# Kernel optimization log

Measured on AMD Instinct MI355X. Metric: run time of the kernel, lower is better.

The kernel has to match this reference:

```python
import jax, jax.numpy as jnp
import numpy as np

NEG_BIG = -1e9


def setup_inputs() -> dict:
    key = jax.random.key(0)
    ks = jax.random.split(key, 6)
    B, Tq, Tv, D, A = 4, 256, 1024, 512, 128
    inputs = jax.random.normal(ks[0], (B, Tv, D), dtype=jnp.float32)
    context = jax.random.normal(ks[1], (B, Tq, D), dtype=jnp.float32)
    mask = jnp.ones((B, Tv), dtype=jnp.int32)  # 1 = valid position
    scale = 1.0 / np.sqrt(D)
    Wk = jax.random.normal(ks[2], (D, A), dtype=jnp.float32) * scale
    bk = jnp.zeros((A,), dtype=jnp.float32)
    Wq = jax.random.normal(ks[3], (D, A), dtype=jnp.float32) * scale
    bq = jnp.zeros((A,), dtype=jnp.float32)
    attn_v = jax.random.normal(ks[4], (A,), dtype=jnp.float32) * (1.0 / np.sqrt(A))
    return {"inputs": inputs, "context": context, "mask": mask,
            "Wk": Wk, "bk": bk, "Wq": Wq, "bq": bq, "attn_v": attn_v}


def reference(inputs, context, mask, Wk, bk, Wq, bq, attn_v):
    # inputs: [B,Tv,D] (keys/values), context: [B,Tq,D] (queries)
    k = jnp.einsum('bvd,da->bva', inputs, Wk) + bk        # [B,Tv,A]
    q = jnp.einsum('bqd,da->bqa', context, Wq) + bq       # [B,Tq,A]
    # additive (Bahdanau) score: sum_a v_a * tanh(q + k)
    t = jnp.tanh(q[:, :, None, :] + k[:, None, :, :])     # [B,Tq,Tv,A]
    scores = jnp.einsum('bqva,a->bqv', t, attn_v)         # [B,Tq,Tv]
    neg = (1.0 - mask.astype(jnp.float32))[:, None, :] * NEG_BIG
    scores = scores + neg
    attn = jax.nn.softmax(scores, axis=-1)                # [B,Tq,Tv]
    return jnp.einsum('bqv,bvd->bqd', attn, inputs)       # [B,Tq,D]
```

## Files before the change

kernel.cpp:

```cpp
#include <hip/hip_runtime.h>
#include <math.h>

#define B   4
#define TQ  256
#define TV  1024
#define D   512
#define A   128

#define LOG2E     1.4426950408889634f
#define TWO_LOG2E 2.8853900817779268f
#define NEG_BIG_F (-1e9f)

#define QBLK (B * TQ / 8)
#define KBLK (B * TV / 8)

__global__ __launch_bounds__(512, 4) void proj_exp_kernel(
    const float* __restrict__ ctx, const float* __restrict__ inp,
    const float* __restrict__ Wq, const float* __restrict__ bq,
    const float* __restrict__ Wk, const float* __restrict__ bk,
    float* __restrict__ Eq, float* __restrict__ EkT) {
  __shared__ float ps[8][8][A];
  __shared__ float es[A][9];

  bool isQ = blockIdx.x < QBLK;
  const float* X; const float* W; const float* bias; int r0;
  if (isQ) { X = ctx; W = Wq; bias = bq; r0 = blockIdx.x * 8; }
  else     { X = inp; W = Wk; bias = bk; r0 = (blockIdx.x - QBLK) * 8; }

  int tid = threadIdx.x;
  int ap = (tid & 63) * 2;
  int g  = tid >> 6;

  int dbase = __builtin_amdgcn_readfirstlane(g * 64);
  const float* Xr = X + (size_t)r0 * D + dbase;
  const float* Wd = W + (size_t)dbase * A + ap;

  float2 acc[8];
#pragma unroll
  for (int j = 0; j < 8; ++j) acc[j] = make_float2(0.f, 0.f);

#pragma unroll 2
  for (int dd = 0; dd < 64; dd += 4) {
    float2 w0 = *(const float2*)(Wd + (size_t)(dd + 0) * A);
    float2 w1 = *(const float2*)(Wd + (size_t)(dd + 1) * A);
    float2 w2 = *(const float2*)(Wd + (size_t)(dd + 2) * A);
    float2 w3 = *(const float2*)(Wd + (size_t)(dd + 3) * A);
    float4 x[8];
#pragma unroll
    for (int j = 0; j < 8; ++j)
      x[j] = *(const float4*)(Xr + (size_t)j * D + dd);
#pragma unroll
    for (int j = 0; j < 8; ++j) {
      acc[j].x = fmaf(x[j].x, w0.x, acc[j].x);
      acc[j].y = fmaf(x[j].x, w0.y, acc[j].y);
      acc[j].x = fmaf(x[j].y, w1.x, acc[j].x);
      acc[j].y = fmaf(x[j].y, w1.y, acc[j].y);
      acc[j].x = fmaf(x[j].z, w2.x, acc[j].x);
      acc[j].y = fmaf(x[j].z, w2.y, acc[j].y);
      acc[j].x = fmaf(x[j].w, w3.x, acc[j].x);
      acc[j].y = fmaf(x[j].w, w3.y, acc[j].y);
    }
  }

#pragma unroll
  for (int j = 0; j < 8; ++j)
    *(float2*)&ps[j][g][ap] = acc[j];
  __syncthreads();

  int j  = tid >> 6;
  int a2 = (tid & 63) * 2;
  float2 s0 = *(const float2*)&ps[j][0][a2];
  float2 s1 = *(const float2*)&ps[j][1][a2];
  float2 s2 = *(const float2*)&ps[j][2][a2];
  float2 s3 = *(const float2*)&ps[j][3][a2];
  float2 s4 = *(const float2*)&ps[j][4][a2];
  float2 s5 = *(const float2*)&ps[j][5][a2];
  float2 s6 = *(const float2*)&ps[j][6][a2];
  float2 s7 = *(const float2*)&ps[j][7][a2];
  float2 bz = *(const float2*)(bias + a2);
  float2 ev;
  ev.x = __builtin_amdgcn_exp2f(
      ((((s0.x + s1.x) + (s2.x + s3.x)) + ((s4.x + s5.x) + (s6.x + s7.x))) + bz.x) * TWO_LOG2E);
  ev.y = __builtin_amdgcn_exp2f(
      ((((s0.y + s1.y) + (s2.y + s3.y)) + ((s4.y + s5.y) + (s6.y + s7.y))) + bz.y) * TWO_LOG2E);

  if (isQ) {
    *(float2*)(Eq + (size_t)(r0 + j) * A + a2) = ev;
  } else {
    es[a2 + 0][j] = ev.x;
    es[a2 + 1][j] = ev.y;
    __syncthreads();
    int b  = r0 >> 10;
    int v0 = r0 & (TV - 1);
    for (int i = tid; i < A * 8; i += 512) {
      int aa = i >> 3, jj = i & 7;
      EkT[((size_t)b * A + aa) * TV + v0 + jj] = es[aa][jj];
    }
  }
}

__global__ __launch_bounds__(1024, 4) void score_softmax_kernel(
    const float* __restrict__ Eq, const float* __restrict__ EkT,
    const float* __restrict__ attn_v, const int* __restrict__ mask,
    float* __restrict__ attn) {
  __shared__ float red[4][16];
  __shared__ float bc[8];

  int tid = threadIdx.x;
  int v0  = tid;
  int xcd = blockIdx.x & 7;
  int b   = xcd & 3;
  int quad = (xcd >> 2) * 32 + (blockIdx.x >> 3);
  int r0  = b * TQ + quad * 4;

  const float* eq0 = Eq + (size_t)(r0 + 0) * A;
  const float* eq1 = Eq + (size_t)(r0 + 1) * A;
  const float* eq2 = Eq + (size_t)(r0 + 2) * A;
  const float* eq3 = Eq + (size_t)(r0 + 3) * A;

  float sumV = 0.f;
#pragma unroll 16
  for (int i = 0; i < A; ++i) sumV += attn_v[i];

  const float* ekb = EkT + (size_t)b * A * TV + v0;
  float t[4] = {0.f, 0.f, 0.f, 0.f};

  float c[4], n[4];
#pragma unroll
  for (int aa = 0; aa < 4; ++aa) c[aa] = ekb[(size_t)aa * TV];

  for (int i = 0; i < A; i += 4) {
    if (i < A - 4) {
#pragma unroll
      for (int aa = 0; aa < 4; ++aa) n[aa] = ekb[(size_t)(i + 4 + aa) * TV];
    }
#pragma unroll
    for (int aa = 0; aa < 4; ++aa) {
      float av = attn_v[i + aa];
      float q0v = eq0[i + aa], q1v = eq1[i + aa];
      float q2v = eq2[i + aa], q3v = eq3[i + aa];
      t[0] = fmaf(av, __builtin_amdgcn_rcpf(fmaf(c[aa], q0v, 1.f)), t[0]);
      t[1] = fmaf(av, __builtin_amdgcn_rcpf(fmaf(c[aa], q1v, 1.f)), t[1]);
      t[2] = fmaf(av, __builtin_amdgcn_rcpf(fmaf(c[aa], q2v, 1.f)), t[2]);
      t[3] = fmaf(av, __builtin_amdgcn_rcpf(fmaf(c[aa], q3v, 1.f)), t[3]);
    }
#pragma unroll
    for (int aa = 0; aa < 4; ++aa) c[aa] = n[aa];
  }

  int mk = mask[b * TV + v0];
  float mkv = (1.f - (float)mk) * NEG_BIG_F;
  float s[4];
#pragma unroll
  for (int r = 0; r < 4; ++r) s[r] = sumV - 2.f * t[r] + mkv;

  float m[4];
#pragma unroll
  for (int r = 0; r < 4; ++r) m[r] = s[r];
  for (int off = 32; off > 0; off >>= 1) {
#pragma unroll
    for (int r = 0; r < 4; ++r) m[r] = fmaxf(m[r], __shfl_down(m[r], off, 64));
  }
  int w = tid >> 6;
  if ((tid & 63) == 0) {
#pragma unroll
    for (int r = 0; r < 4; ++r) red[r][w] = m[r];
  }
  __syncthreads();
  if (tid < 4) {
    float a = red[tid][0];
#pragma unroll
    for (int i = 1; i < 16; ++i) a = fmaxf(a, red[tid][i]);
    bc[tid] = a;
  }
  __syncthreads();
  float M0 = bc[0], M1 = bc[1], M2 = bc[2], M3 = bc[3];

  float e[4];
  e[0] = __builtin_amdgcn_exp2f((s[0] - M0) * LOG2E);
  e[1] = __builtin_amdgcn_exp2f((s[1] - M1) * LOG2E);
  e[2] = __builtin_amdgcn_exp2f((s[2] - M2) * LOG2E);
  e[3] = __builtin_amdgcn_exp2f((s[3] - M3) * LOG2E);
  float l[4];
#pragma unroll
  for (int r = 0; r < 4; ++r) l[r] = e[r];
  for (int off = 32; off > 0; off >>= 1) {
#pragma unroll
    for (int r = 0; r < 4; ++r) l[r] += __shfl_down(l[r], off, 64);
  }
  __syncthreads();
  if ((tid & 63) == 0) {
#pragma unroll
    for (int r = 0; r < 4; ++r) red[r][w] = l[r];
  }
  __syncthreads();
  if (tid < 4) {
    float a = 0.f;
#pragma unroll
    for (int i = 0; i < 16; ++i) a += red[tid][i];
    bc[4 + tid] = a;
  }
  __syncthreads();
  float i0 = 1.f / bc[4], i1 = 1.f / bc[5], i2 = 1.f / bc[6], i3 = 1.f / bc[7];

  attn[(size_t)(r0 + 0) * TV + v0] = e[0] * i0;
  attn[(size_t)(r0 + 1) * TV + v0] = e[1] * i1;
  attn[(size_t)(r0 + 2) * TV + v0] = e[2] * i2;
  attn[(size_t)(r0 + 3) * TV + v0] = e[3] * i3;
}

__global__ __launch_bounds__(512, 4) void pv_kernel(
    const float* __restrict__ attn, const float* __restrict__ X,
    float* __restrict__ out) {
  __shared__ float lds[8 * 1024];
  int gsl = blockIdx.x & 15;
  int b   = gsl & 3;
  int dt  = gsl >> 2;
  int qt  = blockIdx.x >> 4;
  int q0  = b * TQ + qt * 8;
  int tid  = threadIdx.x;
  int w    = tid >> 6;
  int lane = tid & 63;
  int col  = lane & 31;
  int qh   = lane >> 5;
  int d0 = dt * 128 + col * 4;

  float4 acc[4];
#pragma unroll
  for (int j = 0; j < 4; ++j) acc[j] = make_float4(0.f, 0.f, 0.f, 0.f);

  int vbase = w * 128;
  const float* Xb = X + ((size_t)b * TV + vbase) * D + d0;
  const float* arow = attn + (size_t)(q0 + qh * 4) * TV + vbase;

  float4 xc0 = *(const float4*)(Xb + (size_t)0 * D);
  float4 xc1 = *(const float4*)(Xb + (size_t)1 * D);
  float4 xc2 = *(const float4*)(Xb + (size_t)2 * D);
  float4 xc3 = *(const float4*)(Xb + (size_t)3 * D);
  float4 ac[4], an[4];
#pragma unroll
  for (int j = 0; j < 4; ++j)
    ac[j] = *(const float4*)(arow + (size_t)j * TV);

  for (int vi = 0; vi < 128; vi += 4) {
    float4 xn0, xn1, xn2, xn3;
    if (vi < 124) {
      const float* Xn = Xb + (size_t)(vi + 4) * D;
      xn0 = *(const float4*)(Xn + (size_t)0 * D);
      xn1 = *(const float4*)(Xn + (size_t)1 * D);
      xn2 = *(const float4*)(Xn + (size_t)2 * D);
      xn3 = *(const float4*)(Xn + (size_t)3 * D);
#pragma unroll
      for (int j = 0; j < 4; ++j)
        an[j] = *(const float4*)(arow + (size_t)j * TV + vi + 4);
    }
#pragma unroll
    for (int j = 0; j < 4; ++j) {
      float4 av = ac[j];
      acc[j].x = fmaf(av.x, xc0.x, acc[j].x);
      acc[j].y = fmaf(av.x, xc0.y, acc[j].y);
      acc[j].z = fmaf(av.x, xc0.z, acc[j].z);
      acc[j].w = fmaf(av.x, xc0.w, acc[j].w);
      acc[j].x = fmaf(av.y, xc1.x, acc[j].x);
      acc[j].y = fmaf(av.y, xc1.y, acc[j].y);
      acc[j].z = fmaf(av.y, xc1.z, acc[j].z);
      acc[j].w = fmaf(av.y, xc1.w, acc[j].w);
      acc[j].x = fmaf(av.z, xc2.x, acc[j].x);
      acc[j].y = fmaf(av.z, xc2.y, acc[j].y);
      acc[j].z = fmaf(av.z, xc2.z, acc[j].z);
      acc[j].w = fmaf(av.z, xc2.w, acc[j].w);
      acc[j].x = fmaf(av.w, xc3.x, acc[j].x);
      acc[j].y = fmaf(av.w, xc3.y, acc[j].y);
      acc[j].z = fmaf(av.w, xc3.z, acc[j].z);
      acc[j].w = fmaf(av.w, xc3.w, acc[j].w);
    }
    xc0 = xn0; xc1 = xn1; xc2 = xn2; xc3 = xn3;
#pragma unroll
    for (int j = 0; j < 4; ++j) ac[j] = an[j];
  }

  {
    float4* pat = (float4*)lds + (size_t)w * 256;
#pragma unroll
    for (int j = 0; j < 4; ++j)
      pat[(qh * 4 + j) * 32 + col] = acc[j];
  }
  __syncthreads();

  if (tid < 256) {
    int row = tid >> 5;
    int c   = tid & 31;
    const float4* p = (const float4*)lds + tid;
    float4 r = p[0];
#pragma unroll
    for (int i = 1; i < 8; ++i) {
      float4 t = p[(size_t)i * 256];
      r.x += t.x; r.y += t.y; r.z += t.z; r.w += t.w;
    }
    *(float4*)(out + (size_t)(q0 + row) * D + dt * 128 + c * 4) = r;
  }
}

extern "C" void kernel_launch(void* const* d_in, const int* in_sizes, int n_in,
                              void* d_out, int out_size, void* d_ws, size_t ws_size,
                              hipStream_t stream) {
  const float* inputs  = (const float*)d_in[0];
  const float* context = (const float*)d_in[1];
  const int*   mask    = (const int*)d_in[2];
  const float* Wk      = (const float*)d_in[3];
  const float* bk      = (const float*)d_in[4];
  const float* Wq      = (const float*)d_in[5];
  const float* bq      = (const float*)d_in[6];
  const float* attn_v  = (const float*)d_in[7];
  float* out = (float*)d_out;

  float* Eq   = (float*)d_ws;
  float* EkT  = Eq + B * TQ * A;
  float* attn = EkT + (size_t)B * A * TV;

  proj_exp_kernel<<<QBLK + KBLK, 512, 0, stream>>>(context, inputs, Wq, bq,
                                                   Wk, bk, Eq, EkT);
  score_softmax_kernel<<<B * TQ / 4, 1024, 0, stream>>>(Eq, EkT, attn_v, mask,
                                                        attn);
  pv_kernel<<<512, 512, 0, stream>>>(attn, inputs, out);
}
```

Measured before the change: 146.8 us.

## Halve score block threads with float2 per thread; stage attn rows in LDS for PV

The score/softmax kernel now runs 512 threads per block, and each thread handles two adjacent key positions with float2 loads and stores, so every query value it loads feeds twice as many tanh evaluations. The PV kernel copies the block's 8 attention rows into LDS with a cooperative load and then reads them from LDS instead of issuing strided global loads per thread. Risks: the score kernel has fewer waves in flight to hide latency, and the PV kernel adds an extra barrier plus LDS read traffic in its inner loop.

```diff
diff --git a/kernel.cpp b/kernel.cpp
--- a/kernel.cpp
+++ b/kernel.cpp
@@ -99,15 +99,15 @@
   }
 }
 
-__global__ __launch_bounds__(1024, 4) void score_softmax_kernel(
+__global__ __launch_bounds__(512, 4) void score_softmax_kernel(
     const float* __restrict__ Eq, const float* __restrict__ EkT,
     const float* __restrict__ attn_v, const int* __restrict__ mask,
     float* __restrict__ attn) {
-  __shared__ float red[4][16];
+  __shared__ float red[4][8];
   __shared__ float bc[8];
 
   int tid = threadIdx.x;
-  int v0  = tid;
+  int v0  = (tid & 63) * 2 + (tid >> 6) * 128;
   int xcd = blockIdx.x & 7;
   int b   = xcd & 3;
   int quad = (xcd >> 2) * 32 + (blockIdx.x >> 3);
@@ -123,40 +123,54 @@
   for (int i = 0; i < A; ++i) sumV += attn_v[i];
 
   const float* ekb = EkT + (size_t)b * A * TV + v0;
-  float t[4] = {0.f, 0.f, 0.f, 0.f};
-
-  float c[4], n[4];
-#pragma unroll
-  for (int aa = 0; aa < 4; ++aa) c[aa] = ekb[(size_t)aa * TV];
+  float2 t0 = make_float2(0.f, 0.f);
+  float2 t1 = make_float2(0.f, 0.f);
+  float2 t2 = make_float2(0.f, 0.f);
+  float2 t3 = make_float2(0.f, 0.f);
+
+  float2 c0 = *(const float2*)(ekb + (size_t)0 * TV);
+  float2 c1 = *(const float2*)(ekb + (size_t)1 * TV);
+  float2 c2 = *(const float2*)(ekb + (size_t)2 * TV);
+  float2 c3 = *(const float2*)(ekb + (size_t)3 * TV);
 
   for (int i = 0; i < A; i += 4) {
+    float2 n0, n1, n2, n3;
     if (i < A - 4) {
-#pragma unroll
-      for (int aa = 0; aa < 4; ++aa) n[aa] = ekb[(size_t)(i + 4 + aa) * TV];
+      n0 = *(const float2*)(ekb + (size_t)(i + 4) * TV);
+      n1 = *(const float2*)(ekb + (size_t)(i + 5) * TV);
+      n2 = *(const float2*)(ekb + (size_t)(i + 6) * TV);
+      n3 = *(const float2*)(ekb + (size_t)(i + 7) * TV);
     }
 #pragma unroll
     for (int aa = 0; aa < 4; ++aa) {
-      float av = attn_v[i + aa];
+      float2 c = (aa == 0) ? c0 : (aa == 1) ? c1 : (aa == 2) ? c2 : c3;
+      float av  = attn_v[i + aa];
       float q0v = eq0[i + aa], q1v = eq1[i + aa];
       float q2v = eq2[i + aa], q3v = eq3[i + aa];
-      t[0] = fmaf(av, __builtin_amdgcn_rcpf(fmaf(c[aa], q0v, 1.f)), t[0]);
-      t[1] = fmaf(av, __builtin_amdgcn_rcpf(fmaf(c[aa], q1v, 1.f)), t[1]);
-      t[2] = fmaf(av, __builtin_amdgcn_rcpf(fmaf(c[aa], q2v, 1.f)), t[2]);
-      t[3] = fmaf(av, __builtin_amdgcn_rcpf(fmaf(c[aa], q3v, 1.f)), t[3]);
-    }
-#pragma unroll
-    for (int aa = 0; aa < 4; ++aa) c[aa] = n[aa];
-  }
-
-  int mk = mask[b * TV + v0];
-  float mkv = (1.f - (float)mk) * NEG_BIG_F;
-  float s[4];
-#pragma unroll
-  for (int r = 0; r < 4; ++r) s[r] = sumV - 2.f * t[r] + mkv;
+      t0.x = fmaf(av, __builtin_amdgcn_rcpf(fmaf(c.x, q0v, 1.f)), t0.x);
+      t0.y = fmaf(av, __builtin_amdgcn_rcpf(fmaf(c.y, q0v, 1.f)), t0.y);
+      t1.x = fmaf(av, __builtin_amdgcn_rcpf(fmaf(c.x, q1v, 1.f)), t1.x);
+      t1.y = fmaf(av, __builtin_amdgcn_rcpf(fmaf(c.y, q1v, 1.f)), t1.y);
+      t2.x = fmaf(av, __builtin_amdgcn_rcpf(fmaf(c.x, q2v, 1.f)), t2.x);
+      t2.y = fmaf(av, __builtin_amdgcn_rcpf(fmaf(c.y, q2v, 1.f)), t2.y);
+      t3.x = fmaf(av, __builtin_amdgcn_rcpf(fmaf(c.x, q3v, 1.f)), t3.x);
+      t3.y = fmaf(av, __builtin_amdgcn_rcpf(fmaf(c.y, q3v, 1.f)), t3.y);
+    }
+    c0 = n0; c1 = n1; c2 = n2; c3 = n3;
+  }
+
+  int2 mk = *(const int2*)(mask + b * TV + v0);
+  float mkx = (1.f - (float)mk.x) * NEG_BIG_F;
+  float mky = (1.f - (float)mk.y) * NEG_BIG_F;
+  float2 s[4];
+  s[0].x = sumV - 2.f * t0.x + mkx;  s[0].y = sumV - 2.f * t0.y + mky;
+  s[1].x = sumV - 2.f * t1.x + mkx;  s[1].y = sumV - 2.f * t1.y + mky;
+  s[2].x = sumV - 2.f * t2.x + mkx;  s[2].y = sumV - 2.f * t2.y + mky;
+  s[3].x = sumV - 2.f * t3.x + mkx;  s[3].y = sumV - 2.f * t3.y + mky;
 
   float m[4];
 #pragma unroll
-  for (int r = 0; r < 4; ++r) m[r] = s[r];
+  for (int r = 0; r < 4; ++r) m[r] = fmaxf(s[r].x, s[r].y);
   for (int off = 32; off > 0; off >>= 1) {
 #pragma unroll
     for (int r = 0; r < 4; ++r) m[r] = fmaxf(m[r], __shfl_down(m[r], off, 64));
@@ -170,20 +184,20 @@
   if (tid < 4) {
     float a = red[tid][0];
 #pragma unroll
-    for (int i = 1; i < 16; ++i) a = fmaxf(a, red[tid][i]);
+    for (int i = 1; i < 8; ++i) a = fmaxf(a, red[tid][i]);
     bc[tid] = a;
   }
   __syncthreads();
-  float M0 = bc[0], M1 = bc[1], M2 = bc[2], M3 = bc[3];
-
-  float e[4];
-  e[0] = __builtin_amdgcn_exp2f((s[0] - M0) * LOG2E);
-  e[1] = __builtin_amdgcn_exp2f((s[1] - M1) * LOG2E);
-  e[2] = __builtin_amdgcn_exp2f((s[2] - M2) * LOG2E);
-  e[3] = __builtin_amdgcn_exp2f((s[3] - M3) * LOG2E);
+  float M[4] = {bc[0], bc[1], bc[2], bc[3]};
+
+  float2 e[4];
   float l[4];
 #pragma unroll
-  for (int r = 0; r < 4; ++r) l[r] = e[r];
+  for (int r = 0; r < 4; ++r) {
+    e[r].x = __builtin_amdgcn_exp2f((s[r].x - M[r]) * LOG2E);
+    e[r].y = __builtin_amdgcn_exp2f((s[r].y - M[r]) * LOG2E);
+    l[r] = e[r].x + e[r].y;
+  }
   for (int off = 32; off > 0; off >>= 1) {
 #pragma unroll
     for (int r = 0; r < 4; ++r) l[r] += __shfl_down(l[r], off, 64);
@@ -197,16 +211,17 @@
   if (tid < 4) {
     float a = 0.f;
 #pragma unroll
-    for (int i = 0; i < 16; ++i) a += red[tid][i];
+    for (int i = 0; i < 8; ++i) a += red[tid][i];
     bc[4 + tid] = a;
   }
   __syncthreads();
-  float i0 = 1.f / bc[4], i1 = 1.f / bc[5], i2 = 1.f / bc[6], i3 = 1.f / bc[7];
-
-  attn[(size_t)(r0 + 0) * TV + v0] = e[0] * i0;
-  attn[(size_t)(r0 + 1) * TV + v0] = e[1] * i1;
-  attn[(size_t)(r0 + 2) * TV + v0] = e[2] * i2;
-  attn[(size_t)(r0 + 3) * TV + v0] = e[3] * i3;
+
+#pragma unroll
+  for (int r = 0; r < 4; ++r) {
+    float inv = 1.f / bc[4 + r];
+    *(float2*)(attn + (size_t)(r0 + r) * TV + v0) =
+        make_float2(e[r].x * inv, e[r].y * inv);
+  }
 }
 
 __global__ __launch_bounds__(512, 4) void pv_kernel(
@@ -225,22 +240,25 @@
   int qh   = lane >> 5;
   int d0 = dt * 128 + col * 4;
 
+  {
+    const float4* src = (const float4*)(attn + (size_t)q0 * TV);
+    float4* dst = (float4*)lds;
+    for (int i = tid; i < 8 * 256; i += 512) dst[i] = src[i];
+  }
+  __syncthreads();
+
   float4 acc[4];
 #pragma unroll
   for (int j = 0; j < 4; ++j) acc[j] = make_float4(0.f, 0.f, 0.f, 0.f);
 
   int vbase = w * 128;
   const float* Xb = X + ((size_t)b * TV + vbase) * D + d0;
-  const float* arow = attn + (size_t)(q0 + qh * 4) * TV + vbase;
+  const float* arow = &lds[(qh * 4) * 1024 + vbase];
 
   float4 xc0 = *(const float4*)(Xb + (size_t)0 * D);
   float4 xc1 = *(const float4*)(Xb + (size_t)1 * D);
   float4 xc2 = *(const float4*)(Xb + (size_t)2 * D);
   float4 xc3 = *(const float4*)(Xb + (size_t)3 * D);
-  float4 ac[4], an[4];
-#pragma unroll
-  for (int j = 0; j < 4; ++j)
-    ac[j] = *(const float4*)(arow + (size_t)j * TV);
 
   for (int vi = 0; vi < 128; vi += 4) {
     float4 xn0, xn1, xn2, xn3;
@@ -250,13 +268,10 @@
       xn1 = *(const float4*)(Xn + (size_t)1 * D);
       xn2 = *(const float4*)(Xn + (size_t)2 * D);
       xn3 = *(const float4*)(Xn + (size_t)3 * D);
-#pragma unroll
-      for (int j = 0; j < 4; ++j)
-        an[j] = *(const float4*)(arow + (size_t)j * TV + vi + 4);
     }
 #pragma unroll
     for (int j = 0; j < 4; ++j) {
-      float4 av = ac[j];
+      float4 av = *(const float4*)(arow + j * 1024 + vi);
       acc[j].x = fmaf(av.x, xc0.x, acc[j].x);
       acc[j].y = fmaf(av.x, xc0.y, acc[j].y);
       acc[j].z = fmaf(av.x, xc0.z, acc[j].z);
@@ -275,9 +290,9 @@
       acc[j].w = fmaf(av.w, xc3.w, acc[j].w);
     }
     xc0 = xn0; xc1 = xn1; xc2 = xn2; xc3 = xn3;
-#pragma unroll
-    for (int j = 0; j < 4; ++j) ac[j] = an[j];
-  }
+  }
+
+  __syncthreads();
 
   {
     float4* pat = (float4*)lds + (size_t)w * 256;
@@ -320,7 +335,7 @@
 
   proj_exp_kernel<<<QBLK + KBLK, 512, 0, stream>>>(context, inputs, Wq, bq,
                                                    Wk, bk, Eq, EkT);
-  score_softmax_kernel<<<B * TQ / 4, 1024, 0, stream>>>(Eq, EkT, attn_v, mask,
-                                                        attn);
+  score_softmax_kernel<<<B * TQ / 4, 512, 0, stream>>>(Eq, EkT, attn_v, mask,
+                                                       attn);
   pv_kernel<<<512, 512, 0, stream>>>(attn, inputs, out);
 }
```

After: 134.9 us. 8.1% less time.
